# Kernel optimization log

Measured on AMD Instinct MI355X. Metric: run time of the kernel, lower is better.

The kernel has to match this reference:

```python
import jax, jax.numpy as jnp
import numpy as np

D_MODEL = 512
NHEAD = 8
SEQ = 2048
BATCH = 4


def setup_inputs() -> dict:
    key = jax.random.key(0)
    ks = jax.random.split(key, 6)
    s = 0.02
    return {
        "x": jax.random.normal(ks[0], (SEQ, BATCH, D_MODEL), jnp.float32),
        "w_in_g": jax.random.normal(ks[1], (3 * D_MODEL, D_MODEL), jnp.float32) * s,
        "b_in_g": jnp.zeros((3 * D_MODEL,), jnp.float32),
        "w_out_g": jax.random.normal(ks[2], (D_MODEL, D_MODEL), jnp.float32) * s,
        "b_out_g": jnp.zeros((D_MODEL,), jnp.float32),
        "w_in_l": jax.random.normal(ks[3], (3 * D_MODEL, D_MODEL), jnp.float32) * s,
        "b_in_l": jnp.zeros((3 * D_MODEL,), jnp.float32),
        "w_out_l": jax.random.normal(ks[4], (D_MODEL, D_MODEL), jnp.float32) * s,
        "b_out_l": jnp.zeros((D_MODEL,), jnp.float32),
        "local_window_size": 128,
    }


def _mha(x, w_in, b_in, w_out, b_out, nhead):
    # x: (S, B, D); faithful to torch nn.MultiheadAttention (batch_first=False)
    S, B, D = x.shape
    dh = D // nhead
    qkv = x @ w_in.T + b_in                       # (S, B, 3D)
    q, k, v = jnp.split(qkv, 3, axis=-1)
    q = q.reshape(S, B, nhead, dh)
    k = k.reshape(S, B, nhead, dh)
    v = v.reshape(S, B, nhead, dh)
    scores = jnp.einsum("sbhd,tbhd->bhst", q, k) / jnp.sqrt(jnp.float32(dh))
    attn = jax.nn.softmax(scores, axis=-1)        # (B, H, S, S)
    out = jnp.einsum("bhst,tbhd->sbhd", attn, v).reshape(S, B, D)
    return out @ w_out.T + b_out


def reference(x, w_in_g, b_in_g, w_out_g, b_out_g,
              w_in_l, b_in_l, w_out_l, b_out_l, local_window_size):
    S, B, D = x.shape
    W = int(local_window_size)
    global_out = _mha(x, w_in_g, b_in_g, w_out_g, b_out_g, NHEAD)
    # Non-overlapping local windows tile the sequence (S % W == 0 here),
    # so the per-window loop == window-batched attention.
    nW = S // W
    xw = x.reshape(nW, W, B, D).transpose(1, 0, 2, 3).reshape(W, nW * B, D)
    lw = _mha(xw, w_in_l, b_in_l, w_out_l, b_out_l, NHEAD)
    local_out = lw.reshape(W, nW, B, D).transpose(1, 0, 2, 3).reshape(S, B, D)
    return global_out + local_out
```

## Files before the change

### kernel.cpp

```cpp
#include <hip/hip_runtime.h>
#include <hip/hip_bf16.h>
#include <stdint.h>

typedef __attribute__((ext_vector_type(8))) short bf16x8;
typedef __attribute__((ext_vector_type(8))) unsigned short u16x8;
typedef __attribute__((ext_vector_type(4))) float f32x4;

#define DEV __device__ __forceinline__

DEV f32x4 mfma16(bf16x8 a, bf16x8 b, f32x4 c) {
  return __builtin_amdgcn_mfma_f32_16x16x32_bf16(a, b, c, 0, 0, 0);
}

DEV void gload_lds16(const void* g, void* l) {
  __builtin_amdgcn_global_load_lds(
      (__attribute__((address_space(1))) void*)(g),
      (__attribute__((address_space(3))) void*)(l), 16, 0, 0);
}

DEV unsigned short f2bf(float f) {
  __hip_bfloat16 h = __float2bfloat16(f);
  return __builtin_bit_cast(unsigned short, h);
}

__global__ __launch_bounds__(256) void convert_all(
    const float4* __restrict__ s0, const float4* __restrict__ s1,
    const float4* __restrict__ s2, const float4* __restrict__ s3,
    const float4* __restrict__ s4, ushort4* __restrict__ dst)
{
  const int n0 = 1048576, n1 = 196608, n3 = 65536;
  int i = blockIdx.x * 256 + threadIdx.x;
  const float4* s; int off;
  if (i < n0)                 { s = s0; off = 0; }
  else if (i < n0 + n1)       { s = s1; off = n0; }
  else if (i < n0 + 2*n1)     { s = s2; off = n0 + n1; }
  else if (i < n0 + 2*n1+n3)  { s = s3; off = n0 + 2*n1; }
  else                        { s = s4; off = n0 + 2*n1 + n3; }
  float4 v = s[i - off];
  ushort4 o;
  o.x = f2bf(v.x); o.y = f2bf(v.y); o.z = f2bf(v.z); o.w = f2bf(v.w);
  dst[i] = o;
}

#define GEMM_STAGE(Ap, Wp, k0v, bufi)                                          \
  {                                                                            \
    _Pragma("unroll")                                                          \
    for (int is = 0; is < 2; ++is) {                                           \
      const int row = is*64 + (t >> 3);                                        \
      const int slot = (t & 7) ^ (row & 7);                                    \
      gload_lds16((Ap) + (long)(m0 + row)*K + (k0v) + slot*8,                  \
                  (char*)&As[bufi][0] + (is*512 + t)*16);                      \
      gload_lds16((Wp) + (long)(n0 + row)*K + (k0v) + slot*8,                  \
                  (char*)&Ws[bufi][0] + (is*512 + t)*16);                      \
    }                                                                          \
  }

#define GEMM_COMPUTE(cur)                                                      \
  {                                                                            \
    const char* Apl = (const char*)&As[cur][0];                                \
    const char* Wpl = (const char*)&Ws[cur][0];                                \
    __builtin_amdgcn_s_setprio(1);                                             \
    _Pragma("unroll")                                                          \
    for (int kk = 0; kk < 2; ++kk) {                                           \
      bf16x8 af[4], wf[2];                                                     \
      _Pragma("unroll")                                                        \
      for (int i = 0; i < 4; ++i) {                                            \
        const int row = wr*64 + i*16 + l16;                                    \
        const int slot = (kk*4 + g16) ^ (row & 7);                             \
        af[i] = *(const bf16x8*)(Apl + row*128 + slot*16);                     \
      }                                                                        \
      _Pragma("unroll")                                                        \
      for (int j = 0; j < 2; ++j) {                                            \
        const int row = wc*32 + j*16 + l16;                                    \
        const int slot = (kk*4 + g16) ^ (row & 7);                             \
        wf[j] = *(const bf16x8*)(Wpl + row*128 + slot*16);                     \
      }                                                                        \
      _Pragma("unroll")                                                        \
      for (int i = 0; i < 4; ++i)                                              \
        _Pragma("unroll")                                                      \
        for (int j = 0; j < 2; ++j)                                            \
          acc[i][j] = mfma16(af[i], wf[j], acc[i][j]);                         \
    }                                                                          \
    __builtin_amdgcn_s_setprio(0);                                             \
  }

__global__ __launch_bounds__(512) void gemm_qkv(
    const __hip_bfloat16* __restrict__ A0,
    const __hip_bfloat16* __restrict__ Wg, const float* __restrict__ bg,
    const __hip_bfloat16* __restrict__ Wl, const float* __restrict__ bl,
    __hip_bfloat16* __restrict__ qkg, __hip_bfloat16* __restrict__ vtg,
    __hip_bfloat16* __restrict__ qkl, __hip_bfloat16* __restrict__ vtl,
    int M, int N, int K)
{
  __shared__ __attribute__((aligned(16))) char SMEM[65536];
  __hip_bfloat16 (*As)[8192] = (__hip_bfloat16(*)[8192])SMEM;
  __hip_bfloat16 (*Ws)[8192] = (__hip_bfloat16(*)[8192])(SMEM + 32768);
  const int t = threadIdx.x;
  const int lane = t & 63, wid = t >> 6;
  const int g16 = lane >> 4, l16 = lane & 15;
  const int wr = wid >> 2, wc = wid & 3;
  const int bid = blockIdx.x;
  const int xcd = bid & 7, seq = bid >> 3;
  const int sel = xcd >= 4;
  const int xh = xcd & 3;
  const int m0 = (xh*16 + (seq & 15)) * 128;
  const int n0 = (seq >> 4) * 128;
  const __hip_bfloat16* W0 = sel ? Wl : Wg;
  const float* b0 = sel ? bl : bg;
  __hip_bfloat16* qkp = sel ? qkl : qkg;
  __hip_bfloat16* vtp = sel ? vtl : vtg;

  f32x4 acc[4][2] = {};
  const int nks = K >> 6;

  GEMM_STAGE(A0, W0, 0, 0)
  for (int step = 0; step < nks; ++step) {
    const int cur = step & 1;
    if (step + 1 < nks) {
      GEMM_STAGE(A0, W0, (step+1) << 6, cur ^ 1)
      asm volatile("s_waitcnt vmcnt(4)" ::: "memory");
    } else {
      asm volatile("s_waitcnt vmcnt(0)" ::: "memory");
    }
    __builtin_amdgcn_s_barrier();
    asm volatile("" ::: "memory");
    GEMM_COMPUTE(cur)
    asm volatile("" ::: "memory");
    __builtin_amdgcn_s_barrier();
  }

  if (n0 < 1024) {
#pragma unroll
    for (int i = 0; i < 4; ++i) {
      const int gr = m0 + wr*64 + i*16 + g16*4;
#pragma unroll
      for (int j = 0; j < 2; ++j) {
        const int gc = n0 + wc*32 + j*16 + l16;
        const float bias = b0[gc];
        const float scl = (gc >= 512) ? 0.180336880f : 1.0f;
#pragma unroll
        for (int r = 0; r < 4; ++r)
          qkp[(long)(gr + r)*1024 + gc] =
              __float2bfloat16((acc[i][j][r] + bias) * scl);
      }
    }
  } else {
    const int n0l = n0 - 1024;
    short* T = (short*)SMEM;
#pragma unroll
    for (int i = 0; i < 4; ++i) {
      const int sl = wr*16 + i*4 + g16;
#pragma unroll
      for (int j = 0; j < 2; ++j) {
        const int gcl = wc*32 + j*16 + l16;
        const float bias = b0[n0 + gcl];
#pragma unroll
        for (int r = 0; r < 4; ++r)
          T[gcl*136 + r*32 + sl] = (short)f2bf(acc[i][j][r] + bias);
      }
    }
    __syncthreads();
    const int d = t & 127, b4 = t >> 7;
    __hip_bfloat16* dst = vtp + ((long)(b4*512 + n0l + d))*2048 + (m0 >> 2);
#pragma unroll
    for (int k = 0; k < 4; ++k) {
      u16x8 v = *(const u16x8*)(T + d*136 + b4*32 + k*8);
      *(u16x8*)(dst + k*8) = v;
    }
  }
}

__global__ __launch_bounds__(512) void gemm_out(
    const __hip_bfloat16* __restrict__ A0, const __hip_bfloat16* __restrict__ W0,
    const float* __restrict__ b0,
    const __hip_bfloat16* __restrict__ A1, const __hip_bfloat16* __restrict__ W1,
    const float* __restrict__ b1,
    float* __restrict__ Cout, int M, int N, int K)
{
  __shared__ __attribute__((aligned(16))) __hip_bfloat16 As[2][128*64];
  __shared__ __attribute__((aligned(16))) __hip_bfloat16 Ws[2][128*64];
  const int t = threadIdx.x;
  const int lane = t & 63, wid = t >> 6;
  const int g16 = lane >> 4, l16 = lane & 15;
  const int wr = wid >> 2, wc = wid & 3;
  const int lid = blockIdx.x + (blockIdx.y << 6);
  const int xcd = lid & 7, pos = lid >> 3;
  const int m0 = (xcd*8 + (pos & 7)) * 128, n0 = (pos >> 3) * 128;

  f32x4 acc[4][2] = {};
  const int nks = K >> 6;
  const int NS = 2*nks;

  GEMM_STAGE(A0, W0, 0, 0)
  for (int step = 0; step < NS; ++step) {
    const int cur = step & 1;
    if (step + 1 < NS) {
      const int nstep = step + 1;
      const __hip_bfloat16* Ap = (nstep >= nks) ? A1 : A0;
      const __hip_bfloat16* Wp = (nstep >= nks) ? W1 : W0;
      const int k0 = ((nstep >= nks) ? (nstep - nks) : nstep) << 6;
      GEMM_STAGE(Ap, Wp, k0, cur ^ 1)
      asm volatile("s_waitcnt vmcnt(4)" ::: "memory");
    } else {
      asm volatile("s_waitcnt vmcnt(0)" ::: "memory");
    }
    __builtin_amdgcn_s_barrier();
    asm volatile("" ::: "memory");
    GEMM_COMPUTE(cur)
    asm volatile("" ::: "memory");
    __builtin_amdgcn_s_barrier();
  }

#pragma unroll
  for (int i = 0; i < 4; ++i) {
    const int gr = m0 + wr*64 + i*16 + g16*4;
#pragma unroll
    for (int j = 0; j < 2; ++j) {
      const int gc = n0 + wc*32 + j*16 + l16;
      const float bias = b0[gc] + b1[gc];
#pragma unroll
      for (int r = 0; r < 4; ++r)
        Cout[(long)(gr + r)*N + gc] = acc[i][j][r] + bias;
    }
  }
}

__global__ __launch_bounds__(512) void flash_all(
    const __hip_bfloat16* __restrict__ qkg, const __hip_bfloat16* __restrict__ vtg,
    __hip_bfloat16* __restrict__ outg,
    const __hip_bfloat16* __restrict__ qkl, const __hip_bfloat16* __restrict__ vtl,
    __hip_bfloat16* __restrict__ outl,
    const int* __restrict__ wptr, int S, int B, int blkoff)
{
  const int t = threadIdx.x, lane = t & 63, w = t >> 6;
  const int g16 = lane >> 4, l16 = lane & 15;
  const int gid = blockIdx.x + blkoff;
  const int isl = gid >= 512;
  const int id = gid & 511;
  const __hip_bfloat16* qk = isl ? qkl : qkg;
  const __hip_bfloat16* vt = isl ? vtl : vtg;
  __hip_bfloat16* outb = isl ? outl : outg;
  const int Wn = isl ? wptr[0] : S;
  const int xcd = id & 7, seq = id >> 3;
  const int bh = xcd + 8*(seq & 3);
  const int qt = seq >> 2;
  const int b = bh >> 3, h = bh & 7;
  const int q0 = qt * 128;
  const int kv0 = (q0 / Wn) * Wn;
  const int nkt = Wn >> 6;
  const int vtb = bh * 64;

  __shared__ __attribute__((aligned(16))) __hip_bfloat16 Kb[2][64*64];
  __shared__ __attribute__((aligned(16))) __hip_bfloat16 Vb[2][64*64];
  __shared__ __attribute__((aligned(16))) short Pl[8][16*72];

  const int qrow = q0 + w*16 + l16;
  bf16x8 qa[2];
  {
    const __hip_bfloat16* qp = qk + ((long)qrow*B + b)*1024 + h*64 + g16*8;
    qa[0] = *(const bf16x8*)(const void*)qp;
    qa[1] = *(const bf16x8*)(const void*)(qp + 32);
  }
  bf16x8 aones;
#pragma unroll
  for (int e = 0; e < 8; ++e) aones[e] = (short)0x3F80;

  f32x4 o[4] = {};
  f32x4 ol = {};

#define STAGE(tile, bufi)                                                      \
  {                                                                            \
    const int kvs_ = kv0 + (tile)*64;                                          \
    const int row_ = t >> 3;                                                   \
    const int sl_ = (t & 7) ^ (row_ & 7);                                      \
    gload_lds16(qk + ((long)(kvs_+row_)*B + b)*1024 + 512 + h*64 + sl_*8,      \
                (char*)&Kb[bufi][0] + t*16);                                   \
    gload_lds16(vt + (long)(vtb + row_)*2048 + kvs_ + sl_*8,                   \
                (char*)&Vb[bufi][0] + t*16);                                   \
  }

  STAGE(0, 0)

  for (int kt = 0; kt < nkt; ++kt) {
    const int cur = kt & 1;
    if (kt + 1 < nkt) {
      STAGE(kt + 1, cur ^ 1)
      asm volatile("s_waitcnt vmcnt(2)" ::: "memory");
    } else {
      asm volatile("s_waitcnt vmcnt(0)" ::: "memory");
    }
    __builtin_amdgcn_s_barrier();
    asm volatile("" ::: "memory");

    f32x4 s[4] = {};
    const char* Kp = (const char*)&Kb[cur][0];
    __builtin_amdgcn_s_setprio(1);
#pragma unroll
    for (int kk = 0; kk < 2; ++kk)
#pragma unroll
      for (int j = 0; j < 4; ++j) {
        const int row = j*16 + l16;
        const int slot = (kk*4 + g16) ^ (row & 7);
        bf16x8 kf = *(const bf16x8*)(Kp + row*128 + slot*16);
        s[j] = mfma16(kf, qa[kk], s[j]);
      }
    __builtin_amdgcn_s_setprio(0);

    short* Pw = &Pl[w][0];
#pragma unroll
    for (int j = 0; j < 4; ++j) {
      short4 pk4;
      pk4.x = (short)f2bf(__builtin_amdgcn_exp2f(s[j][0]));
      pk4.y = (short)f2bf(__builtin_amdgcn_exp2f(s[j][1]));
      pk4.z = (short)f2bf(__builtin_amdgcn_exp2f(s[j][2]));
      pk4.w = (short)f2bf(__builtin_amdgcn_exp2f(s[j][3]));
      *(short4*)(Pw + l16*72 + j*16 + g16*4) = pk4;
    }

    __builtin_amdgcn_s_setprio(1);
#pragma unroll
    for (int kk = 0; kk < 2; ++kk) {
      bf16x8 pf = *(const bf16x8*)(Pw + l16*72 + kk*32 + g16*8);
      ol = mfma16(aones, pf, ol);
#pragma unroll
      for (int dblk = 0; dblk < 4; ++dblk) {
        const int row = dblk*16 + l16;
        const int slot = (kk*4 + g16) ^ (row & 7);
        bf16x8 vf = *(const bf16x8*)((const char*)&Vb[cur][0] + row*128 + slot*16);
        o[dblk] = mfma16(vf, pf, o[dblk]);
      }
    }
    __builtin_amdgcn_s_setprio(0);

    asm volatile("" ::: "memory");
    __builtin_amdgcn_s_barrier();
  }

  const float inv = 1.f / ol[0];
  const long obase = ((long)qrow*B + b)*512 + h*64;
#pragma unroll
  for (int dblk = 0; dblk < 4; ++dblk) {
    ushort4 pk;
    pk.x = f2bf(o[dblk][0]*inv); pk.y = f2bf(o[dblk][1]*inv);
    pk.z = f2bf(o[dblk][2]*inv); pk.w = f2bf(o[dblk][3]*inv);
    *(ushort4*)(outb + obase + dblk*16 + g16*4) = pk;
  }
}

extern "C" void kernel_launch(void* const* d_in, const int* in_sizes, int n_in,
                              void* d_out, int out_size, void* d_ws, size_t ws_size,
                              hipStream_t stream) {
  const float* x   = (const float*)d_in[0];
  const float* wig = (const float*)d_in[1];
  const float* big = (const float*)d_in[2];
  const float* wog = (const float*)d_in[3];
  const float* bog = (const float*)d_in[4];
  const float* wil = (const float*)d_in[5];
  const float* bil = (const float*)d_in[6];
  const float* wol = (const float*)d_in[7];
  const float* bol = (const float*)d_in[8];
  const int*   wsz = (const int*)d_in[9];

  char* ws = (char*)d_ws;
  __hip_bfloat16* xb    = (__hip_bfloat16*)(ws + 0);
  __hip_bfloat16* wigb  = (__hip_bfloat16*)(ws + 8388608);
  __hip_bfloat16* wilb  = (__hip_bfloat16*)(ws + 9961472);
  __hip_bfloat16* wogb  = (__hip_bfloat16*)(ws + 11534336);
  __hip_bfloat16* wolb  = (__hip_bfloat16*)(ws + 12058624);
  __hip_bfloat16* qkg   = (__hip_bfloat16*)(ws + 12582912);
  __hip_bfloat16* qkl   = (__hip_bfloat16*)(ws + 29360128);
  __hip_bfloat16* vtg   = (__hip_bfloat16*)(ws + 46137344);
  __hip_bfloat16* vtl   = (__hip_bfloat16*)(ws + 54525952);
  __hip_bfloat16* attng = xb;

  const int big_ws = ws_size >= (size_t)71303168;
  __hip_bfloat16* attnl = big_ws ? (__hip_bfloat16*)(ws + 62914560)
                                 : qkg;

  convert_all<<<6144, 256, 0, stream>>>(
      (const float4*)x, (const float4*)wig, (const float4*)wil,
      (const float4*)wog, (const float4*)wol, (ushort4*)ws);

  gemm_qkv<<<1536, 512, 0, stream>>>(xb, wigb, big, wilb, bil,
                                     qkg, vtg, qkl, vtl, 8192, 1536, 512);

  if (big_ws) {
    flash_all<<<1024, 512, 0, stream>>>(qkg, vtg, attng, qkl, vtl, attnl,
                                        wsz, 2048, 4, 0);
  } else {
    flash_all<<<512, 512, 0, stream>>>(qkg, vtg, attng, qkl, vtl, attnl,
                                       wsz, 2048, 4, 0);
    flash_all<<<512, 512, 0, stream>>>(qkg, vtg, attng, qkl, vtl, attnl,
                                       wsz, 2048, 4, 512);
  }

  dim3 go(64, 4);
  gemm_out<<<go, 512, 0, stream>>>(attng, wogb, bog, attnl, wolb, bol,
                                   (float*)d_out, 8192, 512, 512);
}
```

Baseline: 113.5 us.

## Fuse x fp32-to-bf16 conversion into QKV GEMM and halve out-GEMM N tile

The separate conversion of x to bf16 is removed. The QKV GEMM now loads fp32 x straight into registers, converts it and writes bf16 into LDS, overlapping that work with compute on the other buffer. This drops a full write and re-read of the bf16 x copy. Separately, the output GEMM uses 64-wide N tiles with 512 blocks instead of 256, for more parallelism. The cost is more fp32 global traffic per QKV block, since x is re-read by each N-tile column, plus register and VALU conversion work inside the main loop.

```diff
diff --git a/kernel.cpp b/kernel.cpp
--- a/kernel.cpp
+++ b/kernel.cpp
@@ -23,46 +23,32 @@
   return __builtin_bit_cast(unsigned short, h);
 }
 
-__global__ __launch_bounds__(256) void convert_all(
-    const float4* __restrict__ s0, const float4* __restrict__ s1,
-    const float4* __restrict__ s2, const float4* __restrict__ s3,
-    const float4* __restrict__ s4, ushort4* __restrict__ dst)
+__global__ __launch_bounds__(256) void convert_w(
+    const float4* __restrict__ s1, const float4* __restrict__ s2,
+    const float4* __restrict__ s3, const float4* __restrict__ s4,
+    ushort4* __restrict__ dst)
 {
-  const int n0 = 1048576, n1 = 196608, n3 = 65536;
+  const int n1 = 196608, n3 = 65536;
   int i = blockIdx.x * 256 + threadIdx.x;
   const float4* s; int off;
-  if (i < n0)                 { s = s0; off = 0; }
-  else if (i < n0 + n1)       { s = s1; off = n0; }
-  else if (i < n0 + 2*n1)     { s = s2; off = n0 + n1; }
-  else if (i < n0 + 2*n1+n3)  { s = s3; off = n0 + 2*n1; }
-  else                        { s = s4; off = n0 + 2*n1 + n3; }
+  if (i < n1)                 { s = s1; off = 0; }
+  else if (i < 2*n1)          { s = s2; off = n1; }
+  else if (i < 2*n1 + n3)     { s = s3; off = 2*n1; }
+  else                        { s = s4; off = 2*n1 + n3; }
   float4 v = s[i - off];
   ushort4 o;
   o.x = f2bf(v.x); o.y = f2bf(v.y); o.z = f2bf(v.z); o.w = f2bf(v.w);
   dst[i] = o;
 }
 
-#define GEMM_STAGE(Ap, Wp, k0v, bufi)                                          \
-  {                                                                            \
-    _Pragma("unroll")                                                          \
-    for (int is = 0; is < 2; ++is) {                                           \
-      const int row = is*64 + (t >> 3);                                        \
-      const int slot = (t & 7) ^ (row & 7);                                    \
-      gload_lds16((Ap) + (long)(m0 + row)*K + (k0v) + slot*8,                  \
-                  (char*)&As[bufi][0] + (is*512 + t)*16);                      \
-      gload_lds16((Wp) + (long)(n0 + row)*K + (k0v) + slot*8,                  \
-                  (char*)&Ws[bufi][0] + (is*512 + t)*16);                      \
-    }                                                                          \
-  }
-
-#define GEMM_COMPUTE(cur)                                                      \
+#define GEMM_COMPUTE(cur, NJ, WCMUL)                                           \
   {                                                                            \
     const char* Apl = (const char*)&As[cur][0];                                \
     const char* Wpl = (const char*)&Ws[cur][0];                                \
     __builtin_amdgcn_s_setprio(1);                                             \
     _Pragma("unroll")                                                          \
     for (int kk = 0; kk < 2; ++kk) {                                           \
-      bf16x8 af[4], wf[2];                                                     \
+      bf16x8 af[4], wf[NJ];                                                    \
       _Pragma("unroll")                                                        \
       for (int i = 0; i < 4; ++i) {                                            \
         const int row = wr*64 + i*16 + l16;                                    \
@@ -70,22 +56,22 @@
         af[i] = *(const bf16x8*)(Apl + row*128 + slot*16);                     \
       }                                                                        \
       _Pragma("unroll")                                                        \
-      for (int j = 0; j < 2; ++j) {                                            \
-        const int row = wc*32 + j*16 + l16;                                    \
+      for (int j = 0; j < NJ; ++j) {                                           \
+        const int row = wc*WCMUL + j*16 + l16;                                 \
         const int slot = (kk*4 + g16) ^ (row & 7);                             \
         wf[j] = *(const bf16x8*)(Wpl + row*128 + slot*16);                     \
       }                                                                        \
       _Pragma("unroll")                                                        \
       for (int i = 0; i < 4; ++i)                                              \
         _Pragma("unroll")                                                      \
-        for (int j = 0; j < 2; ++j)                                            \
+        for (int j = 0; j < NJ; ++j)                                           \
           acc[i][j] = mfma16(af[i], wf[j], acc[i][j]);                         \
     }                                                                          \
     __builtin_amdgcn_s_setprio(0);                                             \
   }
 
 __global__ __launch_bounds__(512) void gemm_qkv(
-    const __hip_bfloat16* __restrict__ A0,
+    const float* __restrict__ xf,
     const __hip_bfloat16* __restrict__ Wg, const float* __restrict__ bg,
     const __hip_bfloat16* __restrict__ Wl, const float* __restrict__ bl,
     __hip_bfloat16* __restrict__ qkg, __hip_bfloat16* __restrict__ vtg,
@@ -112,20 +98,66 @@
 
   f32x4 acc[4][2] = {};
   const int nks = K >> 6;
-
-  GEMM_STAGE(A0, W0, 0, 0)
+  float4 aA[2], aB[2];
+  int arow[2], aslot[2];
+
+#define QKV_ISSUE_A(k0v)                                                       \
+  {                                                                            \
+    _Pragma("unroll")                                                          \
+    for (int is = 0; is < 2; ++is) {                                           \
+      arow[is] = is*64 + (t >> 3);                                             \
+      aslot[is] = (t & 7) ^ (arow[is] & 7);                                    \
+      const float* ap = xf + (long)(m0 + arow[is])*K + (k0v) + aslot[is]*8;    \
+      aA[is] = *(const float4*)ap;                                             \
+      aB[is] = *(const float4*)(ap + 4);                                       \
+    }                                                                          \
+  }
+
+#define QKV_STAGE_W(k0v, bufi)                                                 \
+  {                                                                            \
+    _Pragma("unroll")                                                          \
+    for (int is = 0; is < 2; ++is) {                                           \
+      const int row = is*64 + (t >> 3);                                        \
+      const int slot = (t & 7) ^ (row & 7);                                    \
+      gload_lds16(W0 + (long)(n0 + row)*K + (k0v) + slot*8,                    \
+                  (char*)&Ws[bufi][0] + (is*512 + t)*16);                      \
+    }                                                                          \
+  }
+
+#define QKV_CVT_WRITE(bufi)                                                    \
+  {                                                                            \
+    _Pragma("unroll")                                                          \
+    for (int is = 0; is < 2; ++is) {                                           \
+      u16x8 pk;                                                                \
+      pk[0] = f2bf(aA[is].x); pk[1] = f2bf(aA[is].y);                          \
+      pk[2] = f2bf(aA[is].z); pk[3] = f2bf(aA[is].w);                          \
+      pk[4] = f2bf(aB[is].x); pk[5] = f2bf(aB[is].y);                          \
+      pk[6] = f2bf(aB[is].z); pk[7] = f2bf(aB[is].w);                          \
+      *(u16x8*)((char*)&As[bufi][0] + (is*512 + t)*16) = pk;                   \
+    }                                                                          \
+  }
+
+  QKV_ISSUE_A(0)
+  QKV_STAGE_W(0, 0)
+  QKV_CVT_WRITE(0)
+  asm volatile("s_waitcnt lgkmcnt(0)" ::: "memory");
+
   for (int step = 0; step < nks; ++step) {
     const int cur = step & 1;
     if (step + 1 < nks) {
-      GEMM_STAGE(A0, W0, (step+1) << 6, cur ^ 1)
-      asm volatile("s_waitcnt vmcnt(4)" ::: "memory");
+      QKV_ISSUE_A((step+1) << 6)
+      QKV_STAGE_W((step+1) << 6, cur ^ 1)
+      asm volatile("s_waitcnt vmcnt(6)" ::: "memory");
     } else {
       asm volatile("s_waitcnt vmcnt(0)" ::: "memory");
     }
     __builtin_amdgcn_s_barrier();
     asm volatile("" ::: "memory");
-    GEMM_COMPUTE(cur)
-    asm volatile("" ::: "memory");
+    GEMM_COMPUTE(cur, 2, 32)
+    if (step + 1 < nks) {
+      QKV_CVT_WRITE(cur ^ 1)
+    }
+    asm volatile("s_waitcnt lgkmcnt(0)" ::: "memory");
     __builtin_amdgcn_s_barrier();
   }
 
@@ -178,20 +210,37 @@
     float* __restrict__ Cout, int M, int N, int K)
 {
   __shared__ __attribute__((aligned(16))) __hip_bfloat16 As[2][128*64];
-  __shared__ __attribute__((aligned(16))) __hip_bfloat16 Ws[2][128*64];
+  __shared__ __attribute__((aligned(16))) __hip_bfloat16 Ws[2][64*64];
   const int t = threadIdx.x;
   const int lane = t & 63, wid = t >> 6;
   const int g16 = lane >> 4, l16 = lane & 15;
   const int wr = wid >> 2, wc = wid & 3;
-  const int lid = blockIdx.x + (blockIdx.y << 6);
-  const int xcd = lid & 7, pos = lid >> 3;
-  const int m0 = (xcd*8 + (pos & 7)) * 128, n0 = (pos >> 3) * 128;
-
-  f32x4 acc[4][2] = {};
+  const int bid = blockIdx.x;
+  const int xcd = bid & 7, pos = bid >> 3;
+  const int m0 = (xcd*8 + (pos & 7)) * 128, n0 = (pos >> 3) * 64;
+
+  f32x4 acc[4][1] = {};
   const int nks = K >> 6;
   const int NS = 2*nks;
 
-  GEMM_STAGE(A0, W0, 0, 0)
+#define OUT_STAGE(Ap, Wp, k0v, bufi)                                           \
+  {                                                                            \
+    _Pragma("unroll")                                                          \
+    for (int is = 0; is < 2; ++is) {                                           \
+      const int row = is*64 + (t >> 3);                                        \
+      const int slot = (t & 7) ^ (row & 7);                                    \
+      gload_lds16((Ap) + (long)(m0 + row)*K + (k0v) + slot*8,                  \
+                  (char*)&As[bufi][0] + (is*512 + t)*16);                      \
+    }                                                                          \
+    {                                                                          \
+      const int row = t >> 3;                                                  \
+      const int slot = (t & 7) ^ (row & 7);                                    \
+      gload_lds16((Wp) + (long)(n0 + row)*K + (k0v) + slot*8,                  \
+                  (char*)&Ws[bufi][0] + t*16);                                 \
+    }                                                                          \
+  }
+
+  OUT_STAGE(A0, W0, 0, 0)
   for (int step = 0; step < NS; ++step) {
     const int cur = step & 1;
     if (step + 1 < NS) {
@@ -199,14 +248,14 @@
       const __hip_bfloat16* Ap = (nstep >= nks) ? A1 : A0;
       const __hip_bfloat16* Wp = (nstep >= nks) ? W1 : W0;
       const int k0 = ((nstep >= nks) ? (nstep - nks) : nstep) << 6;
-      GEMM_STAGE(Ap, Wp, k0, cur ^ 1)
-      asm volatile("s_waitcnt vmcnt(4)" ::: "memory");
+      OUT_STAGE(Ap, Wp, k0, cur ^ 1)
+      asm volatile("s_waitcnt vmcnt(3)" ::: "memory");
     } else {
       asm volatile("s_waitcnt vmcnt(0)" ::: "memory");
     }
     __builtin_amdgcn_s_barrier();
     asm volatile("" ::: "memory");
-    GEMM_COMPUTE(cur)
+    GEMM_COMPUTE(cur, 1, 16)
     asm volatile("" ::: "memory");
     __builtin_amdgcn_s_barrier();
   }
@@ -214,14 +263,11 @@
 #pragma unroll
   for (int i = 0; i < 4; ++i) {
     const int gr = m0 + wr*64 + i*16 + g16*4;
-#pragma unroll
-    for (int j = 0; j < 2; ++j) {
-      const int gc = n0 + wc*32 + j*16 + l16;
-      const float bias = b0[gc] + b1[gc];
-#pragma unroll
-      for (int r = 0; r < 4; ++r)
-        Cout[(long)(gr + r)*N + gc] = acc[i][j][r] + bias;
-    }
+    const int gc = n0 + wc*16 + l16;
+    const float bias = b0[gc] + b1[gc];
+#pragma unroll
+    for (int r = 0; r < 4; ++r)
+      Cout[(long)(gr + r)*N + gc] = acc[i][0][r] + bias;
   }
 }
 
@@ -362,7 +408,6 @@
   const int*   wsz = (const int*)d_in[9];
 
   char* ws = (char*)d_ws;
-  __hip_bfloat16* xb    = (__hip_bfloat16*)(ws + 0);
   __hip_bfloat16* wigb  = (__hip_bfloat16*)(ws + 8388608);
   __hip_bfloat16* wilb  = (__hip_bfloat16*)(ws + 9961472);
   __hip_bfloat16* wogb  = (__hip_bfloat16*)(ws + 11534336);
@@ -371,17 +416,17 @@
   __hip_bfloat16* qkl   = (__hip_bfloat16*)(ws + 29360128);
   __hip_bfloat16* vtg   = (__hip_bfloat16*)(ws + 46137344);
   __hip_bfloat16* vtl   = (__hip_bfloat16*)(ws + 54525952);
-  __hip_bfloat16* attng = xb;
+  __hip_bfloat16* attng = (__hip_bfloat16*)(ws + 0);
 
   const int big_ws = ws_size >= (size_t)71303168;
   __hip_bfloat16* attnl = big_ws ? (__hip_bfloat16*)(ws + 62914560)
                                  : qkg;
 
-  convert_all<<<6144, 256, 0, stream>>>(
-      (const float4*)x, (const float4*)wig, (const float4*)wil,
-      (const float4*)wog, (const float4*)wol, (ushort4*)ws);
-
-  gemm_qkv<<<1536, 512, 0, stream>>>(xb, wigb, big, wilb, bil,
+  convert_w<<<2048, 256, 0, stream>>>(
+      (const float4*)wig, (const float4*)wil,
+      (const float4*)wog, (const float4*)wol, (ushort4*)(ws + 8388608));
+
+  gemm_qkv<<<1536, 512, 0, stream>>>(x, wigb, big, wilb, bil,
                                      qkg, vtg, qkl, vtl, 8192, 1536, 512);
 
   if (big_ws) {
@@ -394,7 +439,6 @@
                                        wsz, 2048, 4, 512);
   }
 
-  dim3 go(64, 4);
-  gemm_out<<<go, 512, 0, stream>>>(attng, wogb, bog, attnl, wolb, bol,
-                                   (float*)d_out, 8192, 512, 512);
-}
+  gemm_out<<<512, 512, 0, stream>>>(attng, wogb, bog, attnl, wolb, bol,
+                                    (float*)d_out, 8192, 512, 512);
+}
```

Measured after the change: 117.6 us. +3.6%, slower.
